# Optimization experiments

Hardware: AMD Instinct MI355X
Metric: run time of the kernel (lower is better)

## Reference

```python
import jax, jax.numpy as jnp
import numpy as np

ND = 3       # ndims
Q = 8        # mixture components
LAT = 64     # latent_dim
N = 2048     # num X points
M = 2048     # num Y points
TRI = ND * (ND + 1) // 2  # 6

_TI, _TJ = np.tril_indices(ND)


def setup_inputs() -> dict:
    key = jax.random.key(0)
    ks = jax.random.split(key, 10)
    s_in = 1.0 / np.sqrt(ND)
    s_lat = 1.0 / np.sqrt(LAT)
    return {
        "x": jax.random.normal(ks[0], (N, ND), jnp.float32),
        "y": jax.random.normal(ks[1], (M, ND), jnp.float32),
        "W1": jax.random.normal(ks[2], (LAT, ND), jnp.float32) * s_in,
        "b1": jax.random.normal(ks[3], (LAT,), jnp.float32) * 0.1,
        "Ww": jax.random.normal(ks[4], (Q, LAT), jnp.float32) * s_lat,
        "bw": jax.random.normal(ks[5], (Q,), jnp.float32) * 0.1,
        "Wf": jax.random.normal(ks[6], (Q * ND, LAT), jnp.float32) * s_lat,
        "bf": jax.random.normal(ks[7], (Q * ND,), jnp.float32) * 0.1,
        "Ws": jax.random.normal(ks[8], (Q * TRI, LAT), jnp.float32) * s_lat,
        "bs": jax.random.normal(ks[9], (Q * TRI,), jnp.float32) * 0.1,
    }


def _features(p, W1, b1, Ww, bw, Wf, bf, Ws, bs):
    # shared hidden layer (computed once per point, unlike the original which
    # recomputes it for each of the 3 heads -- same math)
    h = jax.nn.selu(p @ W1.T + b1)                                  # [n, LAT]
    w = jax.nn.softplus(h @ Ww.T + bw)                              # [n, Q]
    f = jax.nn.softplus(h @ Wf.T + bf).reshape(p.shape[0], Q, ND)   # [n, Q, ND]
    s = jax.nn.softplus(h @ Ws.T + bs).reshape(p.shape[0], Q, TRI)  # [n, Q, TRI]
    # place into lower-triangular L, then A = L @ L.T
    L = jnp.zeros((p.shape[0], Q, ND, ND), p.dtype).at[:, :, _TI, _TJ].set(s)
    A = jnp.einsum('nqab,nqcb->nqac', L, L)                         # [n, Q, ND, ND]
    phase = jnp.einsum('nqd,nd->nq', f, p)                          # [n, Q]
    return w, A, phase


def reference(x, y, W1, b1, Ww, bw, Wf, bf, Ws, bs):
    # __call__ -> k_xy[i, j] = eval(x=Y[j], y=X[i]); shape [N, M]
    wX, AX, phX = _features(x, W1, b1, Ww, bw, Wf, bf, Ws, bs)
    wY, AY, phY = _features(y, W1, b1, Ww, bw, Wf, bf, Ws, bs)

    diff = y[None, :, :] - x[:, None, :]                            # [N, M, ND]
    # r_scaled = diff @ (A_x + A_y) @ diff, split into the two quadratic forms
    qx = jnp.einsum('ijd,iqde,ije->ijq', diff, AX, diff)            # [N, M, Q]
    qy = jnp.einsum('ijd,jqde,ije->ijq', diff, AY, diff)            # [N, M, Q]
    r = qx + qy

    sq5 = jnp.sqrt(jnp.asarray(5.0, r.dtype))
    mat = (1.0 + sq5 * r + (5.0 / 3.0) * r * r) * jnp.exp(-sq5 * r)
    cosine = jnp.cos(2.0 * jnp.pi * (phY[None, :, :] - phX[:, None, :]))
    k = jnp.sum(wY[None, :, :] * wX[:, None, :] * mat * cosine, axis=-1)
    return k
```

## Files before the change

### kernel.cpp

```cpp
#include <hip/hip_runtime.h>
#include <hip/hip_bf16.h>

#define NPTS 2048
#define QMIX 8
#define LATD 64
#define IT   16
#define HIT  8
#define JPB  128

typedef float v2f __attribute__((ext_vector_type(2)));

__device__ __forceinline__ float softplus_f(float x) {
    return fmaxf(x, 0.0f) + log1pf(expf(-fabsf(x)));
}
__device__ __forceinline__ float selu_f(float z) {
    const float sc = 1.0507009873554805f;
    const float sa = 1.7580993408473766f;
    return (z > 0.0f) ? sc * z : sa * expm1f(z);
}

__global__ __launch_bounds__(640) void feat_kernel(
    const float* __restrict__ xin, const float* __restrict__ yin,
    const float* __restrict__ W1, const float* __restrict__ b1,
    const float* __restrict__ Ww, const float* __restrict__ bw,
    const float* __restrict__ Wf, const float* __restrict__ bf,
    const float* __restrict__ Ws, const float* __restrict__ bs,
    float* __restrict__ FX, float* __restrict__ FYI)
{
    __shared__ float hsh[8][LATD + 4];
    __shared__ float raw[8][80];
    const int t = threadIdx.x;

    if (t < 512) {
        const int pl = t & 7, l = t >> 3;
        const int g = blockIdx.x * 8 + pl;
        const bool isx = (g < NPTS);
        const float* pts = isx ? (xin + 3 * g) : (yin + 3 * (g - NPTS));
        const float z = fmaf(W1[l * 3 + 0], pts[0],
                        fmaf(W1[l * 3 + 1], pts[1],
                        fmaf(W1[l * 3 + 2], pts[2], b1[l])));
        hsh[pl][l] = selu_f(z);
    }
    __syncthreads();

    {
        const int o  = t >> 3;
        const int pl = t & 7;
        const int q  = o / 10;
        const int e  = o % 10;
        const float* row;
        float acc;
        if (e == 0)      { row = Ww + q * LATD;                 acc = bw[q]; }
        else if (e <= 3) { row = Wf + (q * 3 + (e - 1)) * LATD; acc = bf[q * 3 + (e - 1)]; }
        else             { row = Ws + (q * 6 + (e - 4)) * LATD; acc = bs[q * 6 + (e - 4)]; }
#pragma unroll
        for (int l4 = 0; l4 < LATD / 4; ++l4) {
            const float4 rv = reinterpret_cast<const float4*>(row)[l4];
            const float4 hv = *reinterpret_cast<const float4*>(&hsh[pl][l4 * 4]);
            acc = fmaf(rv.x, hv.x, acc);
            acc = fmaf(rv.y, hv.y, acc);
            acc = fmaf(rv.z, hv.z, acc);
            acc = fmaf(rv.w, hv.w, acc);
        }
        raw[pl][o] = softplus_f(acc);
    }
    __syncthreads();

    if (t < 64) {
        const int pl2 = t >> 3, q2 = t & 7;
        const int g2  = blockIdx.x * 8 + pl2;
        const bool isx2 = (g2 < NPTS);
        const float* pts2 = isx2 ? (xin + 3 * g2) : (yin + 3 * (g2 - NPTS));
        const float c0 = pts2[0], c1 = pts2[1], c2 = pts2[2];
        const float* r = raw[pl2] + q2 * 10;
        const float w  = r[0];
        const float f0 = r[1], f1 = r[2], f2 = r[3];
        const float s0 = r[4], s1 = r[5], s2 = r[6];
        const float s3 = r[7], s4 = r[8], s5 = r[9];

        const float A00 = s0 * s0;
        const float A11 = fmaf(s1, s1, s2 * s2);
        const float A22 = fmaf(s3, s3, fmaf(s4, s4, s5 * s5));
        const float A01 = s0 * s1;
        const float A02 = s0 * s3;
        const float A12 = fmaf(s1, s3, s2 * s4);
        const float ph  = fmaf(f0, c0, fmaf(f1, c1, f2 * c2));
        float sn, cs;
        sincosf(6.283185307179586477f * ph, &sn, &cs);

        const float EF  = 3.2259751249059600974f;
        const float EF2 = 2.0f * EF;
        const float vals[8] = { EF * A00, EF * A11, EF * A22,
                                EF2 * A01, EF2 * A02, EF2 * A12,
                                w * cs, w * sn };
        if (isx2) {
            float* o = FX + (size_t)g2 * 64 + q2 * 8;
            reinterpret_cast<float4*>(o)[0] = make_float4(vals[0], vals[1], vals[2], vals[3]);
            reinterpret_cast<float4*>(o)[1] = make_float4(vals[4], vals[5], vals[6], vals[7]);
        } else {
            const int pi = g2 - NPTS;
            float* o = FYI + (size_t)(pi >> 1) * 128 + q2 * 16 + (pi & 1);
#pragma unroll
            for (int k = 0; k < 8; ++k) o[k * 2] = vals[k];
        }
    }
}

__global__ __launch_bounds__(256, 4) void pair_kernel(
    const float* __restrict__ xin, const float* __restrict__ yin,
    const float* __restrict__ FX, const float* __restrict__ FYI,
    float* __restrict__ out)
{
    __shared__ float sFX[IT * 64];
    __shared__ v2f   red[HIT][JPB];
    const int t    = threadIdx.x;
    const int wave = t >> 6;
    const int lane = t & 63;
    const int qg   = wave & 1;
    const int jh   = wave >> 1;
    const int jpl  = jh * 64 + lane;
    const int jp   = blockIdx.x * JPB + jpl;
    const int j0   = jp * 2;
    const int i0   = blockIdx.y * IT;

    reinterpret_cast<float4*>(sFX)[t] =
        reinterpret_cast<const float4*>(FX)[i0 * 16 + t];

    v2f fyv[32];
    {
        const float4* fp = reinterpret_cast<const float4*>(
            FYI + (size_t)jp * 128 + qg * 64);
#pragma unroll
        for (int n = 0; n < 16; ++n) {
            const float4 v = fp[n];
            fyv[2 * n + 0] = v2f{v.x, v.y};
            fyv[2 * n + 1] = v2f{v.z, v.w};
        }
    }
    const v2f yc0 = v2f{yin[j0 * 3 + 0], yin[j0 * 3 + 3]};
    const v2f yc1 = v2f{yin[j0 * 3 + 1], yin[j0 * 3 + 4]};
    const v2f yc2 = v2f{yin[j0 * 3 + 2], yin[j0 * 3 + 5]};
    __syncthreads();

    const float P1 = 0.69314718055994530942f;
    const float P2 = 0.16013630893549922444f;

#pragma unroll
    for (int half = 0; half < 2; ++half) {
        v2f acc[HIT];
#pragma unroll
        for (int k = 0; k < HIT; ++k) acc[k] = v2f{0.f, 0.f};

#pragma unroll
        for (int i2 = 0; i2 < HIT; ++i2) {
            const int ii = half * HIT + i2;
            const int i  = i0 + ii;
            const v2f d0 = yc0 - xin[i * 3 + 0];
            const v2f d1 = yc1 - xin[i * 3 + 1];
            const v2f d2 = yc2 - xin[i * 3 + 2];
            const v2f p00 = d0 * d0, p11 = d1 * d1, p22 = d2 * d2;
            const v2f p01 = d0 * d1, p02 = d0 * d2, p12 = d1 * d2;

#pragma unroll
            for (int ql = 0; ql < 4; ++ql) {
                const int q = qg * 4 + ql;
                const float4 ca = *reinterpret_cast<const float4*>(sFX + ii * 64 + q * 8);
                const float4 cb = *reinterpret_cast<const float4*>(sFX + ii * 64 + q * 8 + 4);
                v2f u;
                u  = (fyv[ql * 8 + 0] + ca.x) * p00;
                u += (fyv[ql * 8 + 1] + ca.y) * p11;
                u += (fyv[ql * 8 + 2] + ca.z) * p22;
                u += (fyv[ql * 8 + 3] + ca.w) * p01;
                u += (fyv[ql * 8 + 4] + cb.x) * p02;
                u += (fyv[ql * 8 + 5] + cb.y) * p12;
                const v2f poly = u * (u * P2 + P1) + 1.0f;
                const v2f ex = v2f{__builtin_amdgcn_exp2f(-u.x),
                                   __builtin_amdgcn_exp2f(-u.y)};
                v2f ct = fyv[ql * 8 + 6] * cb.z;
                ct += fyv[ql * 8 + 7] * cb.w;
                acc[i2] += (poly * ex) * ct;
            }
        }

        if (qg == 1) {
#pragma unroll
            for (int i2 = 0; i2 < HIT; ++i2) red[i2][jpl] = acc[i2];
        }
        __syncthreads();
        if (qg == 0) {
#pragma unroll
            for (int i2 = 0; i2 < HIT; ++i2) {
                const v2f s = acc[i2] + red[i2][jpl];
                *reinterpret_cast<float2*>(
                    out + (size_t)(i0 + half * HIT + i2) * NPTS + j0) =
                    make_float2(s.x, s.y);
            }
        }
        __syncthreads();
    }
}

extern "C" void kernel_launch(void* const* d_in, const int* in_sizes, int n_in,
                              void* d_out, int out_size, void* d_ws, size_t ws_size,
                              hipStream_t stream) {
    const float* x  = (const float*)d_in[0];
    const float* y  = (const float*)d_in[1];
    const float* W1 = (const float*)d_in[2];
    const float* b1 = (const float*)d_in[3];
    const float* Ww = (const float*)d_in[4];
    const float* bw = (const float*)d_in[5];
    const float* Wf = (const float*)d_in[6];
    const float* bf = (const float*)d_in[7];
    const float* Ws = (const float*)d_in[8];
    const float* bs = (const float*)d_in[9];
    float* out = (float*)d_out;

    float* FX  = (float*)d_ws;
    float* FYI = FX + (size_t)NPTS * 64;

    feat_kernel<<<dim3((2 * NPTS) / 8), dim3(640), 0, stream>>>(
        x, y, W1, b1, Ww, bw, Wf, bf, Ws, bs, FX, FYI);

    pair_kernel<<<dim3(NPTS / (2 * JPB), NPTS / IT), dim3(256), 0, stream>>>(
        x, y, FX, FYI, out);
}
```

Baseline: 31.51 us.

## Pack mixture components in pairs, one j per lane, read X features via scalar loads

Feature layout changes to a single 72-float stride per point. Mixture components are interleaved in pairs, and the point coordinates are duplicated at the end of each row. In the pair kernel each lane now handles one j, and the packed v2f lanes carry two mixture components instead of two j columns. X-side features are read straight from global memory with wave-uniform addresses (readfirstlane on the wave id), likely as scalar loads, which removes the shared-memory staging and its barrier. The i-tile doubles to 32 rows per block, halving the grid height. The price is more scalar load traffic and more accumulator registers per thread.

```diff
diff --git a/kernel.cpp b/kernel.cpp
--- a/kernel.cpp
+++ b/kernel.cpp
@@ -4,9 +4,9 @@
 #define NPTS 2048
 #define QMIX 8
 #define LATD 64
-#define IT   16
-#define HIT  8
-#define JPB  128
+#define IT   32
+#define HIT  16
+#define FSTRIDE 72
 
 typedef float v2f __attribute__((ext_vector_type(2)));
 
@@ -25,7 +25,7 @@
     const float* __restrict__ Ww, const float* __restrict__ bw,
     const float* __restrict__ Wf, const float* __restrict__ bf,
     const float* __restrict__ Ws, const float* __restrict__ bs,
-    float* __restrict__ FX, float* __restrict__ FYI)
+    float* __restrict__ F)
 {
     __shared__ float hsh[8][LATD + 4];
     __shared__ float raw[8][80];
@@ -93,107 +93,98 @@
         const float vals[8] = { EF * A00, EF * A11, EF * A22,
                                 EF2 * A01, EF2 * A02, EF2 * A12,
                                 w * cs, w * sn };
-        if (isx2) {
-            float* o = FX + (size_t)g2 * 64 + q2 * 8;
-            reinterpret_cast<float4*>(o)[0] = make_float4(vals[0], vals[1], vals[2], vals[3]);
-            reinterpret_cast<float4*>(o)[1] = make_float4(vals[4], vals[5], vals[6], vals[7]);
-        } else {
-            const int pi = g2 - NPTS;
-            float* o = FYI + (size_t)(pi >> 1) * 128 + q2 * 16 + (pi & 1);
-#pragma unroll
-            for (int k = 0; k < 8; ++k) o[k * 2] = vals[k];
+        float* o = F + (size_t)g2 * FSTRIDE;
+        const int base = (q2 >> 1) * 16 + (q2 & 1);
+#pragma unroll
+        for (int k = 0; k < 8; ++k) o[base + k * 2] = vals[k];
+        if (q2 == 0) {
+            o[64] = c0; o[65] = c0;
+            o[66] = c1; o[67] = c1;
+            o[68] = c2; o[69] = c2;
         }
     }
 }
 
 __global__ __launch_bounds__(256, 4) void pair_kernel(
-    const float* __restrict__ xin, const float* __restrict__ yin,
-    const float* __restrict__ FX, const float* __restrict__ FYI,
-    float* __restrict__ out)
+    const float* __restrict__ F, float* __restrict__ out)
 {
-    __shared__ float sFX[IT * 64];
-    __shared__ v2f   red[HIT][JPB];
+    __shared__ float red[HIT][128];
     const int t    = threadIdx.x;
-    const int wave = t >> 6;
+    const int wave = __builtin_amdgcn_readfirstlane(t >> 6);
     const int lane = t & 63;
     const int qg   = wave & 1;
     const int jh   = wave >> 1;
-    const int jpl  = jh * 64 + lane;
-    const int jp   = blockIdx.x * JPB + jpl;
-    const int j0   = jp * 2;
+    const int jl   = jh * 64 + lane;
+    const int j    = blockIdx.x * 128 + jl;
     const int i0   = blockIdx.y * IT;
 
-    reinterpret_cast<float4*>(sFX)[t] =
-        reinterpret_cast<const float4*>(FX)[i0 * 16 + t];
-
-    v2f fyv[32];
+    const float* __restrict__ frow = F + (size_t)(NPTS + j) * FSTRIDE;
+    v2f fy[16];
     {
-        const float4* fp = reinterpret_cast<const float4*>(
-            FYI + (size_t)jp * 128 + qg * 64);
-#pragma unroll
-        for (int n = 0; n < 16; ++n) {
+        const float4* fp = reinterpret_cast<const float4*>(frow + qg * 32);
+#pragma unroll
+        for (int n = 0; n < 8; ++n) {
             const float4 v = fp[n];
-            fyv[2 * n + 0] = v2f{v.x, v.y};
-            fyv[2 * n + 1] = v2f{v.z, v.w};
-        }
-    }
-    const v2f yc0 = v2f{yin[j0 * 3 + 0], yin[j0 * 3 + 3]};
-    const v2f yc1 = v2f{yin[j0 * 3 + 1], yin[j0 * 3 + 4]};
-    const v2f yc2 = v2f{yin[j0 * 3 + 2], yin[j0 * 3 + 5]};
-    __syncthreads();
+            fy[2 * n + 0] = v2f{v.x, v.y};
+            fy[2 * n + 1] = v2f{v.z, v.w};
+        }
+    }
+    const v2f yd0 = *reinterpret_cast<const v2f*>(frow + 64);
+    const v2f yd1 = *reinterpret_cast<const v2f*>(frow + 66);
+    const v2f yd2 = *reinterpret_cast<const v2f*>(frow + 68);
 
     const float P1 = 0.69314718055994530942f;
     const float P2 = 0.16013630893549922444f;
+    const float* __restrict__ fxb = F + (size_t)i0 * FSTRIDE;
 
 #pragma unroll
     for (int half = 0; half < 2; ++half) {
         v2f acc[HIT];
 #pragma unroll
-        for (int k = 0; k < HIT; ++k) acc[k] = v2f{0.f, 0.f};
-
-#pragma unroll
         for (int i2 = 0; i2 < HIT; ++i2) {
-            const int ii = half * HIT + i2;
-            const int i  = i0 + ii;
-            const v2f d0 = yc0 - xin[i * 3 + 0];
-            const v2f d1 = yc1 - xin[i * 3 + 1];
-            const v2f d2 = yc2 - xin[i * 3 + 2];
+            const float* __restrict__ fx = fxb + (half * HIT + i2) * FSTRIDE;
+            const v2f xd0 = *reinterpret_cast<const v2f*>(fx + 64);
+            const v2f xd1 = *reinterpret_cast<const v2f*>(fx + 66);
+            const v2f xd2 = *reinterpret_cast<const v2f*>(fx + 68);
+            const v2f d0 = yd0 - xd0;
+            const v2f d1 = yd1 - xd1;
+            const v2f d2 = yd2 - xd2;
             const v2f p00 = d0 * d0, p11 = d1 * d1, p22 = d2 * d2;
             const v2f p01 = d0 * d1, p02 = d0 * d2, p12 = d1 * d2;
 
-#pragma unroll
-            for (int ql = 0; ql < 4; ++ql) {
-                const int q = qg * 4 + ql;
-                const float4 ca = *reinterpret_cast<const float4*>(sFX + ii * 64 + q * 8);
-                const float4 cb = *reinterpret_cast<const float4*>(sFX + ii * 64 + q * 8 + 4);
+            v2f a = v2f{0.f, 0.f};
+#pragma unroll
+            for (int qpl = 0; qpl < 2; ++qpl) {
+                const v2f* __restrict__ c =
+                    reinterpret_cast<const v2f*>(fx + (qg * 2 + qpl) * 16);
                 v2f u;
-                u  = (fyv[ql * 8 + 0] + ca.x) * p00;
-                u += (fyv[ql * 8 + 1] + ca.y) * p11;
-                u += (fyv[ql * 8 + 2] + ca.z) * p22;
-                u += (fyv[ql * 8 + 3] + ca.w) * p01;
-                u += (fyv[ql * 8 + 4] + cb.x) * p02;
-                u += (fyv[ql * 8 + 5] + cb.y) * p12;
+                u  = (fy[qpl * 8 + 0] + c[0]) * p00;
+                u += (fy[qpl * 8 + 1] + c[1]) * p11;
+                u += (fy[qpl * 8 + 2] + c[2]) * p22;
+                u += (fy[qpl * 8 + 3] + c[3]) * p01;
+                u += (fy[qpl * 8 + 4] + c[4]) * p02;
+                u += (fy[qpl * 8 + 5] + c[5]) * p12;
                 const v2f poly = u * (u * P2 + P1) + 1.0f;
                 const v2f ex = v2f{__builtin_amdgcn_exp2f(-u.x),
                                    __builtin_amdgcn_exp2f(-u.y)};
-                v2f ct = fyv[ql * 8 + 6] * cb.z;
-                ct += fyv[ql * 8 + 7] * cb.w;
-                acc[i2] += (poly * ex) * ct;
+                v2f ct = fy[qpl * 8 + 6] * c[6];
+                ct += fy[qpl * 8 + 7] * c[7];
+                a += (poly * ex) * ct;
             }
+            acc[i2] = a;
         }
 
         if (qg == 1) {
 #pragma unroll
-            for (int i2 = 0; i2 < HIT; ++i2) red[i2][jpl] = acc[i2];
+            for (int i2 = 0; i2 < HIT; ++i2)
+                red[i2][jl] = acc[i2].x + acc[i2].y;
         }
         __syncthreads();
         if (qg == 0) {
 #pragma unroll
             for (int i2 = 0; i2 < HIT; ++i2) {
-                const v2f s = acc[i2] + red[i2][jpl];
-                *reinterpret_cast<float2*>(
-                    out + (size_t)(i0 + half * HIT + i2) * NPTS + j0) =
-                    make_float2(s.x, s.y);
+                out[(size_t)(i0 + half * HIT + i2) * NPTS + j] =
+                    acc[i2].x + acc[i2].y + red[i2][jl];
             }
         }
         __syncthreads();
@@ -215,12 +206,10 @@
     const float* bs = (const float*)d_in[9];
     float* out = (float*)d_out;
 
-    float* FX  = (float*)d_ws;
-    float* FYI = FX + (size_t)NPTS * 64;
+    float* F = (float*)d_ws;
 
     feat_kernel<<<dim3((2 * NPTS) / 8), dim3(640), 0, stream>>>(
-        x, y, W1, b1, Ww, bw, Wf, bf, Ws, bs, FX, FYI);
-
-    pair_kernel<<<dim3(NPTS / (2 * JPB), NPTS / IT), dim3(256), 0, stream>>>(
-        x, y, FX, FYI, out);
-}
+        x, y, W1, b1, Ww, bw, Wf, bf, Ws, bs, F);
+
+    pair_kernel<<<dim3(NPTS / 128, NPTS / IT), dim3(256), 0, stream>>>(F, out);
+}
```

New measurement: 34.24 us. +8.7%, slower.

## Split mixture components across four waves and read X features via scalar loads

Applied to the files above, without the earlier changes.

Restructures the pair kernel so the four waves of a block each handle two mixture components for the same 64 column pairs, combining partial sums through a three-way shared-memory reduction. X features are no longer staged in shared memory. They are read straight from global memory with wave-uniform addresses, which allows scalar loads, and the point coordinates are packed into the feature rows. The row tile grows to 32 and the phase loop is no longer unrolled. This trades fewer registers per thread and no LDS staging for more reduction traffic and more global reads of the Y feature rows.

```diff
diff --git a/kernel.cpp b/kernel.cpp
--- a/kernel.cpp
+++ b/kernel.cpp
@@ -4,9 +4,11 @@
 #define NPTS 2048
 #define QMIX 8
 #define LATD 64
-#define IT   16
+#define IT   32
 #define HIT  8
-#define JPB  128
+#define NPH  (IT / HIT)
+#define FXS  72
+#define FYS  136
 
 typedef float v2f __attribute__((ext_vector_type(2)));
 
@@ -94,105 +96,103 @@
                                 EF2 * A01, EF2 * A02, EF2 * A12,
                                 w * cs, w * sn };
         if (isx2) {
-            float* o = FX + (size_t)g2 * 64 + q2 * 8;
+            float* o = FX + (size_t)g2 * FXS + q2 * 8;
             reinterpret_cast<float4*>(o)[0] = make_float4(vals[0], vals[1], vals[2], vals[3]);
             reinterpret_cast<float4*>(o)[1] = make_float4(vals[4], vals[5], vals[6], vals[7]);
+            if (q2 == 0) {
+                float* oc = FX + (size_t)g2 * FXS + 64;
+                oc[0] = c0; oc[1] = c1; oc[2] = c2;
+            }
         } else {
             const int pi = g2 - NPTS;
-            float* o = FYI + (size_t)(pi >> 1) * 128 + q2 * 16 + (pi & 1);
+            float* o = FYI + (size_t)(pi >> 1) * FYS + q2 * 16 + (pi & 1);
 #pragma unroll
             for (int k = 0; k < 8; ++k) o[k * 2] = vals[k];
+            if (q2 == 0) {
+                float* oc = FYI + (size_t)(pi >> 1) * FYS + 128 + (pi & 1);
+                oc[0] = c0; oc[2] = c1; oc[4] = c2;
+            }
         }
     }
 }
 
 __global__ __launch_bounds__(256, 4) void pair_kernel(
-    const float* __restrict__ xin, const float* __restrict__ yin,
     const float* __restrict__ FX, const float* __restrict__ FYI,
     float* __restrict__ out)
 {
-    __shared__ float sFX[IT * 64];
-    __shared__ v2f   red[HIT][JPB];
+    __shared__ v2f red[3][HIT][64];
     const int t    = threadIdx.x;
-    const int wave = t >> 6;
+    const int qg   = __builtin_amdgcn_readfirstlane(t >> 6);
     const int lane = t & 63;
-    const int qg   = wave & 1;
-    const int jh   = wave >> 1;
-    const int jpl  = jh * 64 + lane;
-    const int jp   = blockIdx.x * JPB + jpl;
+    const int jp   = blockIdx.x * 64 + lane;
     const int j0   = jp * 2;
     const int i0   = blockIdx.y * IT;
 
-    reinterpret_cast<float4*>(sFX)[t] =
-        reinterpret_cast<const float4*>(FX)[i0 * 16 + t];
-
-    v2f fyv[32];
+    const float* __restrict__ frow = FYI + (size_t)jp * FYS;
+    v2f fy[16];
     {
-        const float4* fp = reinterpret_cast<const float4*>(
-            FYI + (size_t)jp * 128 + qg * 64);
-#pragma unroll
-        for (int n = 0; n < 16; ++n) {
-            const float4 v = fp[n];
-            fyv[2 * n + 0] = v2f{v.x, v.y};
-            fyv[2 * n + 1] = v2f{v.z, v.w};
-        }
-    }
-    const v2f yc0 = v2f{yin[j0 * 3 + 0], yin[j0 * 3 + 3]};
-    const v2f yc1 = v2f{yin[j0 * 3 + 1], yin[j0 * 3 + 4]};
-    const v2f yc2 = v2f{yin[j0 * 3 + 2], yin[j0 * 3 + 5]};
-    __syncthreads();
+        const float4* fp = reinterpret_cast<const float4*>(frow + qg * 32);
+#pragma unroll
+        for (int m = 0; m < 8; ++m) {
+            const float4 v = fp[m];
+            fy[2 * m + 0] = v2f{v.x, v.y};
+            fy[2 * m + 1] = v2f{v.z, v.w};
+        }
+    }
+    const v2f yc0 = *reinterpret_cast<const v2f*>(frow + 128);
+    const v2f yc1 = *reinterpret_cast<const v2f*>(frow + 130);
+    const v2f yc2 = *reinterpret_cast<const v2f*>(frow + 132);
 
     const float P1 = 0.69314718055994530942f;
     const float P2 = 0.16013630893549922444f;
 
-#pragma unroll
-    for (int half = 0; half < 2; ++half) {
+    for (int ph = 0; ph < NPH; ++ph) {
         v2f acc[HIT];
 #pragma unroll
-        for (int k = 0; k < HIT; ++k) acc[k] = v2f{0.f, 0.f};
+        for (int i2 = 0; i2 < HIT; ++i2) acc[i2] = v2f{0.f, 0.f};
 
 #pragma unroll
         for (int i2 = 0; i2 < HIT; ++i2) {
-            const int ii = half * HIT + i2;
-            const int i  = i0 + ii;
-            const v2f d0 = yc0 - xin[i * 3 + 0];
-            const v2f d1 = yc1 - xin[i * 3 + 1];
-            const v2f d2 = yc2 - xin[i * 3 + 2];
+            const float* __restrict__ fx =
+                FX + (size_t)(i0 + ph * HIT + i2) * FXS;
+            const float x0 = fx[64], x1 = fx[65], x2 = fx[66];
+            const v2f d0 = yc0 - x0;
+            const v2f d1 = yc1 - x1;
+            const v2f d2 = yc2 - x2;
             const v2f p00 = d0 * d0, p11 = d1 * d1, p22 = d2 * d2;
             const v2f p01 = d0 * d1, p02 = d0 * d2, p12 = d1 * d2;
 
 #pragma unroll
-            for (int ql = 0; ql < 4; ++ql) {
-                const int q = qg * 4 + ql;
-                const float4 ca = *reinterpret_cast<const float4*>(sFX + ii * 64 + q * 8);
-                const float4 cb = *reinterpret_cast<const float4*>(sFX + ii * 64 + q * 8 + 4);
+            for (int ql = 0; ql < 2; ++ql) {
+                const float* __restrict__ c = fx + (qg * 2 + ql) * 8;
                 v2f u;
-                u  = (fyv[ql * 8 + 0] + ca.x) * p00;
-                u += (fyv[ql * 8 + 1] + ca.y) * p11;
-                u += (fyv[ql * 8 + 2] + ca.z) * p22;
-                u += (fyv[ql * 8 + 3] + ca.w) * p01;
-                u += (fyv[ql * 8 + 4] + cb.x) * p02;
-                u += (fyv[ql * 8 + 5] + cb.y) * p12;
+                u  = (fy[ql * 8 + 0] + c[0]) * p00;
+                u += (fy[ql * 8 + 1] + c[1]) * p11;
+                u += (fy[ql * 8 + 2] + c[2]) * p22;
+                u += (fy[ql * 8 + 3] + c[3]) * p01;
+                u += (fy[ql * 8 + 4] + c[4]) * p02;
+                u += (fy[ql * 8 + 5] + c[5]) * p12;
                 const v2f poly = u * (u * P2 + P1) + 1.0f;
                 const v2f ex = v2f{__builtin_amdgcn_exp2f(-u.x),
                                    __builtin_amdgcn_exp2f(-u.y)};
-                v2f ct = fyv[ql * 8 + 6] * cb.z;
-                ct += fyv[ql * 8 + 7] * cb.w;
+                v2f ct = fy[ql * 8 + 6] * c[6];
+                ct += fy[ql * 8 + 7] * c[7];
                 acc[i2] += (poly * ex) * ct;
             }
         }
 
-        if (qg == 1) {
-#pragma unroll
-            for (int i2 = 0; i2 < HIT; ++i2) red[i2][jpl] = acc[i2];
+        if (qg != 0) {
+#pragma unroll
+            for (int i2 = 0; i2 < HIT; ++i2) red[qg - 1][i2][lane] = acc[i2];
         }
         __syncthreads();
         if (qg == 0) {
 #pragma unroll
             for (int i2 = 0; i2 < HIT; ++i2) {
-                const v2f s = acc[i2] + red[i2][jpl];
+                const v2f s = acc[i2] + red[0][i2][lane]
+                            + red[1][i2][lane] + red[2][i2][lane];
                 *reinterpret_cast<float2*>(
-                    out + (size_t)(i0 + half * HIT + i2) * NPTS + j0) =
+                    out + (size_t)(i0 + ph * HIT + i2) * NPTS + j0) =
                     make_float2(s.x, s.y);
             }
         }
@@ -216,11 +216,11 @@
     float* out = (float*)d_out;
 
     float* FX  = (float*)d_ws;
-    float* FYI = FX + (size_t)NPTS * 64;
+    float* FYI = FX + (size_t)NPTS * FXS;
 
     feat_kernel<<<dim3((2 * NPTS) / 8), dim3(640), 0, stream>>>(
         x, y, W1, b1, Ww, bw, Wf, bf, Ws, bs, FX, FYI);
 
-    pair_kernel<<<dim3(NPTS / (2 * JPB), NPTS / IT), dim3(256), 0, stream>>>(
-        x, y, FX, FYI, out);
-}
+    pair_kernel<<<dim3(NPTS / 128, NPTS / IT), dim3(256), 0, stream>>>(
+        FX, FYI, out);
+}
```

Result: slower. 34.20 us (+8.6%).
